# Kernel tuning notes

Hardware: AMD Instinct MI355X
Metric: run time of the kernel (lower is better)

Reference implementation:

```python
import jax, jax.numpy as jnp
import numpy as np

T, H, E, F = 2048, 1024, 32, 512   # tokens, hidden, routed experts, moe intermediate
K, NG, TG = 8, 8, 4                # top_k, n_group, topk_group
FS = 1024                          # shared-expert intermediate = n_shared(2) * F
SCALE = 2.5                        # routed_scaling_factor


def _silu_and_mul(gu):
    g, u = jnp.split(gu, 2, axis=-1)
    return jax.nn.silu(g) * u


def _route(x, gate_w, bias):
    # DeepSeek-V3 noaux_tc grouped top-k with correction bias (sigmoid scores)
    logits = x @ gate_w.T                                   # [T,E]
    scores = jax.nn.sigmoid(logits.astype(jnp.float32))
    sc = scores + bias[None, :]                             # biased scores, selection only
    n_tok = sc.shape[0]
    grp = sc.reshape(n_tok, NG, E // NG)
    top2, _ = jax.lax.top_k(grp, 2)
    group_scores = top2.sum(-1)                             # [T,NG]
    _, gidx = jax.lax.top_k(group_scores, TG)
    gmask = jnp.zeros((n_tok, NG), scores.dtype).at[jnp.arange(n_tok)[:, None], gidx].set(1.0)
    emask = jnp.repeat(gmask, E // NG, axis=1)              # [T,E]
    masked = jnp.where(emask > 0, sc, -jnp.inf)
    _, topk_idx = jax.lax.top_k(masked, K)                  # [T,K]
    w = jnp.take_along_axis(scores, topk_idx, axis=1)       # unbiased scores as weights
    w = w / (w.sum(-1, keepdims=True) + 1e-20)              # renormalize (norm_topk_prob)
    return w, topk_idx


def _forward(x, gate_w, corr_bias, w_gate_up, w_down, shared_gate_up, shared_down):
    w, idx = _route(x, gate_w, corr_bias)
    # dense grouped-GEMM reference: every expert on every token, sparse combine
    gu = jnp.einsum('th,egh->teg', x, w_gate_up)            # [T,E,2F]
    h = _silu_and_mul(gu)                                   # [T,E,F]
    y = jnp.einsum('tef,ehf->teh', h, w_down)               # [T,E,H]
    n_tok = x.shape[0]
    combine = jnp.zeros((n_tok, E), x.dtype).at[jnp.arange(n_tok)[:, None], idx].add(w.astype(x.dtype))
    routed = jnp.einsum('te,teh->th', combine, y) * SCALE
    shared = _silu_and_mul(x @ shared_gate_up.T) @ shared_down.T
    return routed + shared


def setup_inputs() -> dict:
    key = jax.random.key(0)
    ks = jax.random.split(key, 7)
    return {
        "hidden_states": jax.random.normal(ks[0], (T, H), jnp.float32),
        "gate_w": jax.random.normal(ks[1], (E, H), jnp.float32) * 0.02,
        "corr_bias": jax.random.normal(ks[2], (E,), jnp.float32) * 0.01,
        "w_gate_up": jax.random.normal(ks[3], (E, 2 * F, H), jnp.float32) * 0.02,
        "w_down": jax.random.normal(ks[4], (E, H, F), jnp.float32) * 0.02,
        "shared_gate_up": jax.random.normal(ks[5], (2 * FS, H), jnp.float32) * 0.02,
        "shared_down": jax.random.normal(ks[6], (H, FS), jnp.float32) * 0.02,
        "num_global_tokens": T,
        "max_num_tokens_per_gpu": T,
    }


def reference(hidden_states, gate_w, corr_bias, w_gate_up, w_down, shared_gate_up, shared_down, num_global_tokens, max_num_tokens_per_gpu):
    return _forward(hidden_states, gate_w, corr_bias, w_gate_up, w_down, shared_gate_up, shared_down)
```

## Files before the change

### kernel.cpp

```cpp
#include <hip/hip_runtime.h>
#include <hip/hip_bf16.h>

#define T_TOK 2048
#define H_DIM 1024
#define E_EXP 32
#define F_DIM 512
#define FS_DIM 1024
#define K_TOP 8
#define NGRP 8
#define TGRP 4
#define GSZ (E_EXP / NGRP)
#define RSCALE 2.5f
#define CAP 2048

typedef short  short8 __attribute__((ext_vector_type(8)));
typedef __bf16 bf16x4 __attribute__((ext_vector_type(4)));
typedef float  f32x4  __attribute__((ext_vector_type(4)));

__global__ void cvt_f32_bf16(const float* __restrict__ src, __bf16* __restrict__ dst, int n4) {
  int i = blockIdx.x * blockDim.x + threadIdx.x;
  const int stride = gridDim.x * blockDim.x;
  for (; i < n4; i += stride) {
    const float4 v = reinterpret_cast<const float4*>(src)[i];
    bf16x4 o;
    o[0] = (__bf16)v.x; o[1] = (__bf16)v.y; o[2] = (__bf16)v.z; o[3] = (__bf16)v.w;
    reinterpret_cast<bf16x4*>(dst)[i] = o;
  }
}

__global__ __launch_bounds__(64) void route_kernel(
    const float* __restrict__ x, const float* __restrict__ gw,
    const float* __restrict__ bias, int* __restrict__ tk_idx, float* __restrict__ tk_w) {
  const int t = blockIdx.x;
  const int lane = threadIdx.x;
  float xr[16];
#pragma unroll
  for (int i = 0; i < 16; i++) xr[i] = x[t * H_DIM + i * 64 + lane];
  float sc[E_EXP];
#pragma unroll
  for (int e = 0; e < E_EXP; e++) {
    const float* w = gw + e * H_DIM;
    float s = 0.f;
#pragma unroll
    for (int i = 0; i < 16; i++) s += xr[i] * w[i * 64 + lane];
#pragma unroll
    for (int off = 32; off > 0; off >>= 1) s += __shfl_xor(s, off);
    sc[e] = 1.f / (1.f + expf(-s));
  }
  if (lane == 0) {
    float b[E_EXP];
    for (int e = 0; e < E_EXP; e++) b[e] = sc[e] + bias[e];
    float gs[NGRP];
    for (int g = 0; g < NGRP; g++) {
      float m1 = -1e30f, m2 = -1e30f;
      for (int j = 0; j < GSZ; j++) {
        float v = b[g * GSZ + j];
        if (v > m1) { m2 = m1; m1 = v; } else if (v > m2) { m2 = v; }
      }
      gs[g] = m1 + m2;
    }
    unsigned gmask = 0;
    for (int it = 0; it < TGRP; it++) {
      float best = -1e30f; int bi = 0;
      for (int g = 0; g < NGRP; g++)
        if (!((gmask >> g) & 1) && gs[g] > best) { best = gs[g]; bi = g; }
      gmask |= 1u << bi;
    }
    unsigned emask = 0; float wsum = 0.f;
    int idx8[K_TOP];
    for (int it = 0; it < K_TOP; it++) {
      float best = -1e30f; int bi = 0;
      for (int e = 0; e < E_EXP; e++) {
        if (!((gmask >> (e / GSZ)) & 1)) continue;
        if ((emask >> e) & 1) continue;
        if (b[e] > best) { best = b[e]; bi = e; }
      }
      emask |= 1u << bi;
      idx8[it] = bi;
      wsum += sc[bi];
    }
    const float inv = 1.f / (wsum + 1e-20f);
    for (int k = 0; k < K_TOP; k++) {
      tk_idx[t * K_TOP + k] = idx8[k];
      tk_w[t * K_TOP + k] = sc[idx8[k]] * inv;
    }
  }
}

__global__ void scatter_kernel(const int* __restrict__ tk_idx, int* __restrict__ counts,
                               int* __restrict__ recs) {
  const int i = blockIdx.x * blockDim.x + threadIdx.x;
  if (i >= T_TOK * K_TOP) return;
  const int e = tk_idx[i];
  const int pos = atomicAdd(&counts[e], 1);
  recs[e * CAP + pos] = i;
}

__global__ void offsets_kernel(const int* __restrict__ counts, int* __restrict__ offs) {
  if (threadIdx.x == 0) {
    int a = 0;
    for (int e = 0; e < E_EXP; e++) { offs[e] = a; a += counts[e]; }
  }
}

#define BM 128
#define BN 128
#define BK 64

constexpr int MODE_GU = 0, MODE_DOWN = 1, MODE_SGU = 2, MODE_SDOWN = 3;

__device__ __forceinline__ void gload_lds16(const void* g, void* l) {
  __builtin_amdgcn_global_load_lds(
      (__attribute__((address_space(1))) const void*)g,
      (__attribute__((address_space(3))) void*)l, 16, 0, 0);
}

template <int MODE>
__global__ __launch_bounds__(256) void gemm_kernel(
    const __bf16* __restrict__ Abase, const __bf16* __restrict__ Bbase,
    void* __restrict__ Out,
    const int* __restrict__ recs, const int* __restrict__ counts,
    const int* __restrict__ offs, const float* __restrict__ tk_w) {

  constexpr int K = (MODE == MODE_DOWN) ? F_DIM : ((MODE == MODE_SDOWN) ? FS_DIM : H_DIM);

  const int e = (MODE == MODE_GU || MODE == MODE_DOWN) ? blockIdx.z : 0;
  const int m0 = blockIdx.y * BM;
  int count = T_TOK, off_e = 0;
  if (MODE == MODE_GU || MODE == MODE_DOWN) {
    count = counts[e];
    off_e = offs[e];
    if (m0 >= count) return;
  }
  const int tid = threadIdx.x, wid = tid >> 6, lane = tid & 63;

  __shared__ __align__(16) __bf16 As[BM * BK];
  __shared__ __align__(16) __bf16 Bs[BN * BK];

  const int colk = (lane & 7) * 8;
  const __bf16* aptr[4];
  const __bf16* bptr[4];
#pragma unroll
  for (int i = 0; i < 4; i++) {
    const int row = wid * 32 + i * 8 + (lane >> 3);
    if (MODE == MODE_GU) {
      int r = m0 + row; if (r > count - 1) r = count - 1;
      const int rec = recs[e * CAP + r];
      aptr[i] = Abase + (size_t)(rec >> 3) * H_DIM + colk;
    } else if (MODE == MODE_DOWN) {
      int r = m0 + row; if (r > count - 1) r = count - 1;
      aptr[i] = Abase + (size_t)(off_e + r) * F_DIM + colk;
    } else {
      aptr[i] = Abase + (size_t)(m0 + row) * K + colk;
    }
    int brow;
    if (MODE == MODE_GU)       brow = (row < 64) ? (blockIdx.x * 64 + row) : (F_DIM + blockIdx.x * 64 + row - 64);
    else if (MODE == MODE_SGU) brow = (row < 64) ? (blockIdx.x * 64 + row) : (FS_DIM + blockIdx.x * 64 + row - 64);
    else                       brow = blockIdx.x * BN + row;
    const __bf16* bexp = Bbase +
        ((MODE == MODE_GU)   ? (size_t)e * 2 * F_DIM * H_DIM :
         (MODE == MODE_DOWN) ? (size_t)e * H_DIM * F_DIM : (size_t)0);
    bptr[i] = bexp + (size_t)brow * K + colk;
  }

  f32x4 acc[2][8];
#pragma unroll
  for (int a = 0; a < 2; a++)
#pragma unroll
    for (int b = 0; b < 8; b++) acc[a][b] = f32x4{0.f, 0.f, 0.f, 0.f};

  const int lr = lane & 15, lh = lane >> 4;

  for (int k0 = 0; k0 < K; k0 += BK) {
#pragma unroll
    for (int i = 0; i < 4; i++)
      gload_lds16(aptr[i] + k0, (char*)As + (wid * 4 + i) * 1024);
#pragma unroll
    for (int i = 0; i < 4; i++)
      gload_lds16(bptr[i] + k0, (char*)Bs + (wid * 4 + i) * 1024);
    __syncthreads();
#pragma unroll
    for (int kk = 0; kk < 2; kk++) {
      short8 af[2], bfr[8];
#pragma unroll
      for (int fm = 0; fm < 2; fm++)
        af[fm] = *reinterpret_cast<const short8*>(&As[(wid * 32 + fm * 16 + lr) * BK + kk * 32 + lh * 8]);
#pragma unroll
      for (int fn = 0; fn < 8; fn++)
        bfr[fn] = *reinterpret_cast<const short8*>(&Bs[(fn * 16 + lr) * BK + kk * 32 + lh * 8]);
#pragma unroll
      for (int fn = 0; fn < 8; fn++)
#pragma unroll
        for (int fm = 0; fm < 2; fm++)
          acc[fm][fn] = __builtin_amdgcn_mfma_f32_16x16x32_bf16(af[fm], bfr[fn], acc[fm][fn], 0, 0, 0);
    }
    __syncthreads();
  }

  if (MODE == MODE_GU) {
    __bf16* h_out = (__bf16*)Out;
#pragma unroll
    for (int fm = 0; fm < 2; fm++)
#pragma unroll
      for (int j = 0; j < 4; j++) {
        const int row = wid * 32 + fm * 16 + lh * 4 + j;
        if (m0 + row < count) {
#pragma unroll
          for (int fn = 0; fn < 4; fn++) {
            const float g = acc[fm][fn][j], u = acc[fm][fn + 4][j];
            const float hv = g / (1.f + expf(-g)) * u;
            const int f = blockIdx.x * 64 + fn * 16 + lr;
            h_out[(size_t)(off_e + m0 + row) * F_DIM + f] = (__bf16)hv;
          }
        }
      }
  } else if (MODE == MODE_SGU) {
    __bf16* h_out = (__bf16*)Out;
#pragma unroll
    for (int fm = 0; fm < 2; fm++)
#pragma unroll
      for (int j = 0; j < 4; j++) {
        const int row = wid * 32 + fm * 16 + lh * 4 + j;
#pragma unroll
        for (int fn = 0; fn < 4; fn++) {
          const float g = acc[fm][fn][j], u = acc[fm][fn + 4][j];
          const float hv = g / (1.f + expf(-g)) * u;
          const int f = blockIdx.x * 64 + fn * 16 + lr;
          h_out[(size_t)(m0 + row) * FS_DIM + f] = (__bf16)hv;
        }
      }
  } else if (MODE == MODE_DOWN) {
    float* y = (float*)Out;
#pragma unroll
    for (int fm = 0; fm < 2; fm++)
#pragma unroll
      for (int j = 0; j < 4; j++) {
        const int row = wid * 32 + fm * 16 + lh * 4 + j;
        if (m0 + row < count) {
          const int rec = recs[e * CAP + m0 + row];
          const float w = tk_w[rec];
          const size_t base = (size_t)rec * H_DIM + blockIdx.x * BN;
#pragma unroll
          for (int fn = 0; fn < 8; fn++)
            y[base + fn * 16 + lr] = acc[fm][fn][j] * w;
        }
      }
  } else {
    float* o = (float*)Out;
#pragma unroll
    for (int fm = 0; fm < 2; fm++)
#pragma unroll
      for (int j = 0; j < 4; j++) {
        const int row = wid * 32 + fm * 16 + lh * 4 + j;
#pragma unroll
        for (int fn = 0; fn < 8; fn++)
          o[(size_t)(m0 + row) * H_DIM + blockIdx.x * BN + fn * 16 + lr] = acc[fm][fn][j];
      }
  }
}

__global__ void combine_kernel(const float* __restrict__ y_slot, float* __restrict__ out) {
  const int gid = blockIdx.x * blockDim.x + threadIdx.x;
  const int t = gid >> 8;
  const int c0 = (gid & 255) * 4;
  float4 s = {0.f, 0.f, 0.f, 0.f};
#pragma unroll
  for (int k = 0; k < K_TOP; k++) {
    const float4 v = *reinterpret_cast<const float4*>(&y_slot[((size_t)t * K_TOP + k) * H_DIM + c0]);
    s.x += v.x; s.y += v.y; s.z += v.z; s.w += v.w;
  }
  float4 o = *reinterpret_cast<float4*>(&out[(size_t)t * H_DIM + c0]);
  o.x += RSCALE * s.x; o.y += RSCALE * s.y; o.z += RSCALE * s.z; o.w += RSCALE * s.w;
  *reinterpret_cast<float4*>(&out[(size_t)t * H_DIM + c0]) = o;
}

extern "C" void kernel_launch(void* const* d_in, const int* in_sizes, int n_in,
                              void* d_out, int out_size, void* d_ws, size_t ws_size,
                              hipStream_t stream) {
  const float* x    = (const float*)d_in[0];
  const float* gw   = (const float*)d_in[1];
  const float* bias = (const float*)d_in[2];
  const float* wgu  = (const float*)d_in[3];
  const float* wd   = (const float*)d_in[4];
  const float* sgu  = (const float*)d_in[5];
  const float* sd   = (const float*)d_in[6];

  char* ws = (char*)d_ws;
  size_t o = 0;
  auto alloc = [&](size_t bytes) {
    char* p = ws + o;
    o += (bytes + 255) & ~(size_t)255;
    return (void*)p;
  };
  __bf16* xb     = (__bf16*)alloc((size_t)T_TOK * H_DIM * 2);
  __bf16* wgub   = (__bf16*)alloc((size_t)E_EXP * 2 * F_DIM * H_DIM * 2);
  __bf16* wdb    = (__bf16*)alloc((size_t)E_EXP * H_DIM * F_DIM * 2);
  __bf16* sgub   = (__bf16*)alloc((size_t)2 * FS_DIM * H_DIM * 2);
  __bf16* sdb    = (__bf16*)alloc((size_t)H_DIM * FS_DIM * 2);
  __bf16* h_buf  = (__bf16*)alloc((size_t)T_TOK * K_TOP * F_DIM * 2);
  float*  y_slot = (float*) alloc((size_t)T_TOK * K_TOP * H_DIM * 4);
  __bf16* hs     = (__bf16*)alloc((size_t)T_TOK * FS_DIM * 2);
  int*   tk_idx  = (int*)  alloc((size_t)T_TOK * K_TOP * 4);
  float* tk_w    = (float*)alloc((size_t)T_TOK * K_TOP * 4);
  int*   counts  = (int*)  alloc((size_t)E_EXP * 4);
  int*   offs    = (int*)  alloc((size_t)E_EXP * 4);
  int*   recs    = (int*)  alloc((size_t)E_EXP * CAP * 4);
  if (o > ws_size) return;

  cvt_f32_bf16<<<2048, 256, 0, stream>>>(x,   xb,   T_TOK * H_DIM / 4);
  cvt_f32_bf16<<<2048, 256, 0, stream>>>(wgu, wgub, E_EXP * 2 * F_DIM * H_DIM / 4);
  cvt_f32_bf16<<<2048, 256, 0, stream>>>(wd,  wdb,  E_EXP * H_DIM * F_DIM / 4);
  cvt_f32_bf16<<<2048, 256, 0, stream>>>(sgu, sgub, 2 * FS_DIM * H_DIM / 4);
  cvt_f32_bf16<<<1024, 256, 0, stream>>>(sd,  sdb,  H_DIM * FS_DIM / 4);

  route_kernel<<<T_TOK, 64, 0, stream>>>(x, gw, bias, tk_idx, tk_w);

  hipMemsetAsync(counts, 0, E_EXP * 4, stream);
  scatter_kernel<<<(T_TOK * K_TOP + 255) / 256, 256, 0, stream>>>(tk_idx, counts, recs);
  offsets_kernel<<<1, 64, 0, stream>>>(counts, offs);

  gemm_kernel<MODE_GU>   <<<dim3(F_DIM / 64, T_TOK / BM, E_EXP), 256, 0, stream>>>(xb, wgub, h_buf, recs, counts, offs, tk_w);
  gemm_kernel<MODE_DOWN> <<<dim3(H_DIM / BN, T_TOK / BM, E_EXP), 256, 0, stream>>>(h_buf, wdb, y_slot, recs, counts, offs, tk_w);
  gemm_kernel<MODE_SGU>  <<<dim3(FS_DIM / 64, T_TOK / BM, 1), 256, 0, stream>>>(xb, sgub, hs, recs, counts, offs, tk_w);
  gemm_kernel<MODE_SDOWN><<<dim3(H_DIM / BN, T_TOK / BM, 1), 256, 0, stream>>>(hs, sdb, d_out, recs, counts, offs, tk_w);

  combine_kernel<<<T_TOK * H_DIM / 4 / 256, 256, 0, stream>>>(y_slot, (float*)d_out);
}
```

Measured before the change: 318.8 us.

## Use 256x256 double-buffered tiles for routed expert GEMMs

Adds a separate 512-thread kernel for the routed gate-up and down GEMMs that uses 256x256 output tiles with an 8-wave 2x4 layout. It double-buffers the LDS tiles so the next K-slice loads while MFMAs run on the current one. The larger tiles are meant to raise arithmetic intensity and cut the number of blocks that reload the same weights. The shared-expert GEMMs keep the original 128x128 kernel. The cost is 128KB of LDS per block and heavy register pressure, which limits occupancy, and experts with few tokens may waste more work on partial tiles.

```diff
diff --git a/kernel.cpp b/kernel.cpp
--- a/kernel.cpp
+++ b/kernel.cpp
@@ -103,11 +103,7 @@
   }
 }
 
-#define BM 128
-#define BN 128
 #define BK 64
-
-constexpr int MODE_GU = 0, MODE_DOWN = 1, MODE_SGU = 2, MODE_SDOWN = 3;
 
 __device__ __forceinline__ void gload_lds16(const void* g, void* l) {
   __builtin_amdgcn_global_load_lds(
@@ -116,26 +112,25 @@
 }
 
 template <int MODE>
-__global__ __launch_bounds__(256) void gemm_kernel(
+__global__ __launch_bounds__(512, 2) void gemm256_kernel(
     const __bf16* __restrict__ Abase, const __bf16* __restrict__ Bbase,
     void* __restrict__ Out,
     const int* __restrict__ recs, const int* __restrict__ counts,
     const int* __restrict__ offs, const float* __restrict__ tk_w) {
 
-  constexpr int K = (MODE == MODE_DOWN) ? F_DIM : ((MODE == MODE_SDOWN) ? FS_DIM : H_DIM);
-
-  const int e = (MODE == MODE_GU || MODE == MODE_DOWN) ? blockIdx.z : 0;
-  const int m0 = blockIdx.y * BM;
-  int count = T_TOK, off_e = 0;
-  if (MODE == MODE_GU || MODE == MODE_DOWN) {
-    count = counts[e];
-    off_e = offs[e];
-    if (m0 >= count) return;
-  }
+  constexpr int K = (MODE == 0) ? H_DIM : F_DIM;
+  const int e = blockIdx.z;
+  const int m0 = blockIdx.y * 256;
+  const int count = counts[e];
+  const int off_e = offs[e];
+  if (m0 >= count) return;
+  const int bx = blockIdx.x;
   const int tid = threadIdx.x, wid = tid >> 6, lane = tid & 63;
-
-  __shared__ __align__(16) __bf16 As[BM * BK];
-  __shared__ __align__(16) __bf16 Bs[BN * BK];
+  const int wr = wid >> 2, wc = wid & 3;
+  const int lr = lane & 15, lh = lane >> 4;
+
+  __shared__ __align__(16) __bf16 As[2][256 * BK];
+  __shared__ __align__(16) __bf16 Bs[2][256 * BK];
 
   const int colk = (lane & 7) * 8;
   const __bf16* aptr[4];
@@ -143,24 +138,133 @@
 #pragma unroll
   for (int i = 0; i < 4; i++) {
     const int row = wid * 32 + i * 8 + (lane >> 3);
-    if (MODE == MODE_GU) {
-      int r = m0 + row; if (r > count - 1) r = count - 1;
+    int r = m0 + row; if (r > count - 1) r = count - 1;
+    if (MODE == 0) {
       const int rec = recs[e * CAP + r];
       aptr[i] = Abase + (size_t)(rec >> 3) * H_DIM + colk;
-    } else if (MODE == MODE_DOWN) {
-      int r = m0 + row; if (r > count - 1) r = count - 1;
+    } else {
       aptr[i] = Abase + (size_t)(off_e + r) * F_DIM + colk;
+    }
+    int brow;
+    if (MODE == 0) {
+      const int sub = row & 63, wcb = row >> 6;
+      const int f = bx * 128 + wcb * 32 + (sub & 31);
+      brow = (sub < 32) ? f : (F_DIM + f);
+      bptr[i] = Bbase + (size_t)e * 2 * F_DIM * H_DIM + (size_t)brow * H_DIM + colk;
     } else {
-      aptr[i] = Abase + (size_t)(m0 + row) * K + colk;
-    }
+      brow = bx * 256 + row;
+      bptr[i] = Bbase + (size_t)e * H_DIM * F_DIM + (size_t)brow * F_DIM + colk;
+    }
+  }
+
+  f32x4 acc[8][4];
+#pragma unroll
+  for (int a = 0; a < 8; a++)
+#pragma unroll
+    for (int b = 0; b < 4; b++) acc[a][b] = f32x4{0.f, 0.f, 0.f, 0.f};
+
+  constexpr int NT = K / BK;
+
+#pragma unroll
+  for (int i = 0; i < 4; i++) {
+    gload_lds16(aptr[i], (char*)&As[0][0] + (wid * 32 + i * 8) * 128);
+    gload_lds16(bptr[i], (char*)&Bs[0][0] + (wid * 32 + i * 8) * 128);
+  }
+  __syncthreads();
+
+  int cur = 0;
+  for (int t = 0; t < NT; ++t) {
+    if (t + 1 < NT) {
+      const int k0 = (t + 1) * BK;
+#pragma unroll
+      for (int i = 0; i < 4; i++) {
+        gload_lds16(aptr[i] + k0, (char*)&As[cur ^ 1][0] + (wid * 32 + i * 8) * 128);
+        gload_lds16(bptr[i] + k0, (char*)&Bs[cur ^ 1][0] + (wid * 32 + i * 8) * 128);
+      }
+    }
+#pragma unroll
+    for (int kk = 0; kk < 2; kk++) {
+      short8 af[8], bfr[4];
+#pragma unroll
+      for (int fm = 0; fm < 8; fm++)
+        af[fm] = *reinterpret_cast<const short8*>(&As[cur][(wr * 128 + fm * 16 + lr) * BK + kk * 32 + lh * 8]);
+#pragma unroll
+      for (int fn = 0; fn < 4; fn++)
+        bfr[fn] = *reinterpret_cast<const short8*>(&Bs[cur][(wc * 64 + fn * 16 + lr) * BK + kk * 32 + lh * 8]);
+#pragma unroll
+      for (int fn = 0; fn < 4; fn++)
+#pragma unroll
+        for (int fm = 0; fm < 8; fm++)
+          acc[fm][fn] = __builtin_amdgcn_mfma_f32_16x16x32_bf16(af[fm], bfr[fn], acc[fm][fn], 0, 0, 0);
+    }
+    __syncthreads();
+    cur ^= 1;
+  }
+
+  if (MODE == 0) {
+    __bf16* h_out = (__bf16*)Out;
+#pragma unroll
+    for (int fm = 0; fm < 8; fm++)
+#pragma unroll
+      for (int j = 0; j < 4; j++) {
+        const int row = wr * 128 + fm * 16 + lh * 4 + j;
+        if (m0 + row < count) {
+#pragma unroll
+          for (int fn = 0; fn < 2; fn++) {
+            const float g = acc[fm][fn][j], u = acc[fm][fn + 2][j];
+            const float hv = g / (1.f + expf(-g)) * u;
+            const int f = bx * 128 + wc * 32 + fn * 16 + lr;
+            h_out[(size_t)(off_e + m0 + row) * F_DIM + f] = (__bf16)hv;
+          }
+        }
+      }
+  } else {
+    float* y = (float*)Out;
+#pragma unroll
+    for (int fm = 0; fm < 8; fm++)
+#pragma unroll
+      for (int j = 0; j < 4; j++) {
+        const int row = wr * 128 + fm * 16 + lh * 4 + j;
+        if (m0 + row < count) {
+          const int rec = recs[e * CAP + m0 + row];
+          const float w = tk_w[rec];
+          const size_t base = (size_t)rec * H_DIM + bx * 256;
+#pragma unroll
+          for (int fn = 0; fn < 4; fn++)
+            y[base + wc * 64 + fn * 16 + lr] = acc[fm][fn][j] * w;
+        }
+      }
+  }
+}
+
+#define BM 128
+#define BN 128
+
+constexpr int MODE_SGU = 2, MODE_SDOWN = 3;
+
+template <int MODE>
+__global__ __launch_bounds__(256) void gemm_kernel(
+    const __bf16* __restrict__ Abase, const __bf16* __restrict__ Bbase,
+    void* __restrict__ Out) {
+
+  constexpr int K = (MODE == MODE_SDOWN) ? FS_DIM : H_DIM;
+  const int m0 = blockIdx.y * BM;
+  const int tid = threadIdx.x, wid = tid >> 6, lane = tid & 63;
+
+  __shared__ __align__(16) __bf16 As[BM * BK];
+  __shared__ __align__(16) __bf16 Bs[BN * BK];
+
+  const int colk = (lane & 7) * 8;
+  const __bf16* aptr[4];
+  const __bf16* bptr[4];
+#pragma unroll
+  for (int i = 0; i < 4; i++) {
+    const int row = wid * 32 + i * 8 + (lane >> 3);
+    aptr[i] = Abase + (size_t)(m0 + row) * K + colk;
     int brow;
-    if (MODE == MODE_GU)       brow = (row < 64) ? (blockIdx.x * 64 + row) : (F_DIM + blockIdx.x * 64 + row - 64);
-    else if (MODE == MODE_SGU) brow = (row < 64) ? (blockIdx.x * 64 + row) : (FS_DIM + blockIdx.x * 64 + row - 64);
-    else                       brow = blockIdx.x * BN + row;
-    const __bf16* bexp = Bbase +
-        ((MODE == MODE_GU)   ? (size_t)e * 2 * F_DIM * H_DIM :
-         (MODE == MODE_DOWN) ? (size_t)e * H_DIM * F_DIM : (size_t)0);
-    bptr[i] = bexp + (size_t)brow * K + colk;
+    if (MODE == MODE_SGU) brow = (row < 64) ? (blockIdx.x * 64 + row) : (FS_DIM + blockIdx.x * 64 + row - 64);
+    else                  brow = blockIdx.x * BN + row;
+    bptr[i] = Bbase + (size_t)brow * K + colk;
   }
 
   f32x4 acc[2][8];
@@ -197,24 +301,7 @@
     __syncthreads();
   }
 
-  if (MODE == MODE_GU) {
-    __bf16* h_out = (__bf16*)Out;
-#pragma unroll
-    for (int fm = 0; fm < 2; fm++)
-#pragma unroll
-      for (int j = 0; j < 4; j++) {
-        const int row = wid * 32 + fm * 16 + lh * 4 + j;
-        if (m0 + row < count) {
-#pragma unroll
-          for (int fn = 0; fn < 4; fn++) {
-            const float g = acc[fm][fn][j], u = acc[fm][fn + 4][j];
-            const float hv = g / (1.f + expf(-g)) * u;
-            const int f = blockIdx.x * 64 + fn * 16 + lr;
-            h_out[(size_t)(off_e + m0 + row) * F_DIM + f] = (__bf16)hv;
-          }
-        }
-      }
-  } else if (MODE == MODE_SGU) {
+  if (MODE == MODE_SGU) {
     __bf16* h_out = (__bf16*)Out;
 #pragma unroll
     for (int fm = 0; fm < 2; fm++)
@@ -227,22 +314,6 @@
           const float hv = g / (1.f + expf(-g)) * u;
           const int f = blockIdx.x * 64 + fn * 16 + lr;
           h_out[(size_t)(m0 + row) * FS_DIM + f] = (__bf16)hv;
-        }
-      }
-  } else if (MODE == MODE_DOWN) {
-    float* y = (float*)Out;
-#pragma unroll
-    for (int fm = 0; fm < 2; fm++)
-#pragma unroll
-      for (int j = 0; j < 4; j++) {
-        const int row = wid * 32 + fm * 16 + lh * 4 + j;
-        if (m0 + row < count) {
-          const int rec = recs[e * CAP + m0 + row];
-          const float w = tk_w[rec];
-          const size_t base = (size_t)rec * H_DIM + blockIdx.x * BN;
-#pragma unroll
-          for (int fn = 0; fn < 8; fn++)
-            y[base + fn * 16 + lr] = acc[fm][fn][j] * w;
         }
       }
   } else {
@@ -319,10 +390,10 @@
   scatter_kernel<<<(T_TOK * K_TOP + 255) / 256, 256, 0, stream>>>(tk_idx, counts, recs);
   offsets_kernel<<<1, 64, 0, stream>>>(counts, offs);
 
-  gemm_kernel<MODE_GU>   <<<dim3(F_DIM / 64, T_TOK / BM, E_EXP), 256, 0, stream>>>(xb, wgub, h_buf, recs, counts, offs, tk_w);
-  gemm_kernel<MODE_DOWN> <<<dim3(H_DIM / BN, T_TOK / BM, E_EXP), 256, 0, stream>>>(h_buf, wdb, y_slot, recs, counts, offs, tk_w);
-  gemm_kernel<MODE_SGU>  <<<dim3(FS_DIM / 64, T_TOK / BM, 1), 256, 0, stream>>>(xb, sgub, hs, recs, counts, offs, tk_w);
-  gemm_kernel<MODE_SDOWN><<<dim3(H_DIM / BN, T_TOK / BM, 1), 256, 0, stream>>>(hs, sdb, d_out, recs, counts, offs, tk_w);
+  gemm256_kernel<0><<<dim3(2 * F_DIM / 256, CAP / 256, E_EXP), 512, 0, stream>>>(xb, wgub, h_buf, recs, counts, offs, tk_w);
+  gemm256_kernel<1><<<dim3(H_DIM / 256, CAP / 256, E_EXP), 512, 0, stream>>>(h_buf, wdb, y_slot, recs, counts, offs, tk_w);
+  gemm_kernel<MODE_SGU>  <<<dim3(FS_DIM / 64, T_TOK / BM), 256, 0, stream>>>(xb, sgub, hs);
+  gemm_kernel<MODE_SDOWN><<<dim3(H_DIM / BN, T_TOK / BM), 256, 0, stream>>>(hs, sdb, d_out);
 
   combine_kernel<<<T_TOK * H_DIM / 4 / 256, 256, 0, stream>>>(y_slot, (float*)d_out);
 }
```

Result: slower. 557.0 us (+74.7%).

## Merge routed and shared GEMMs into shared launches and fold scatter into routing

Applied to the files above, without the earlier changes.

Combines the five conversion launches into one kernel and moves the x conversion into the routing kernel. The expert scatter (atomic counts and record lists) now happens inside routing, which removes the scatter and offsets kernels; each GEMM block instead computes its prefix offset from the counts. Routed and shared-expert GEMMs run in the same launch per phase by using extra z slices, so the dense shared work can fill gaps left by the uneven expert tiles. The cost is more branching inside the GEMM, a prefix sum per block, and atomics issued by one lane per token.

```diff
diff --git a/kernel.cpp b/kernel.cpp
--- a/kernel.cpp
+++ b/kernel.cpp
@@ -17,10 +17,24 @@
 typedef __bf16 bf16x4 __attribute__((ext_vector_type(4)));
 typedef float  f32x4  __attribute__((ext_vector_type(4)));
 
-__global__ void cvt_f32_bf16(const float* __restrict__ src, __bf16* __restrict__ dst, int n4) {
-  int i = blockIdx.x * blockDim.x + threadIdx.x;
+__global__ void cvt_all(const float* __restrict__ s0, __bf16* __restrict__ d0, int n0,
+                        const float* __restrict__ s1, __bf16* __restrict__ d1, int n1,
+                        const float* __restrict__ s2, __bf16* __restrict__ d2, int n2,
+                        const float* __restrict__ s3, __bf16* __restrict__ d3, int n3) {
+  const int ntot = n0 + n1 + n2 + n3;
+  int gid = blockIdx.x * blockDim.x + threadIdx.x;
   const int stride = gridDim.x * blockDim.x;
-  for (; i < n4; i += stride) {
+  for (; gid < ntot; gid += stride) {
+    int i = gid;
+    const float* src; __bf16* dst;
+    if (i < n0) { src = s0; dst = d0; }
+    else { i -= n0;
+      if (i < n1) { src = s1; dst = d1; }
+      else { i -= n1;
+        if (i < n2) { src = s2; dst = d2; }
+        else { i -= n2; src = s3; dst = d3; }
+      }
+    }
     const float4 v = reinterpret_cast<const float4*>(src)[i];
     bf16x4 o;
     o[0] = (__bf16)v.x; o[1] = (__bf16)v.y; o[2] = (__bf16)v.z; o[3] = (__bf16)v.w;
@@ -30,12 +44,15 @@
 
 __global__ __launch_bounds__(64) void route_kernel(
     const float* __restrict__ x, const float* __restrict__ gw,
-    const float* __restrict__ bias, int* __restrict__ tk_idx, float* __restrict__ tk_w) {
+    const float* __restrict__ bias, float* __restrict__ tk_w,
+    int* __restrict__ counts, int* __restrict__ recs, __bf16* __restrict__ xb) {
   const int t = blockIdx.x;
   const int lane = threadIdx.x;
   float xr[16];
 #pragma unroll
   for (int i = 0; i < 16; i++) xr[i] = x[t * H_DIM + i * 64 + lane];
+#pragma unroll
+  for (int i = 0; i < 16; i++) xb[t * H_DIM + i * 64 + lane] = (__bf16)xr[i];
   float sc[E_EXP];
 #pragma unroll
   for (int e = 0; e < E_EXP; e++) {
@@ -81,33 +98,17 @@
     }
     const float inv = 1.f / (wsum + 1e-20f);
     for (int k = 0; k < K_TOP; k++) {
-      tk_idx[t * K_TOP + k] = idx8[k];
-      tk_w[t * K_TOP + k] = sc[idx8[k]] * inv;
-    }
-  }
-}
-
-__global__ void scatter_kernel(const int* __restrict__ tk_idx, int* __restrict__ counts,
-                               int* __restrict__ recs) {
-  const int i = blockIdx.x * blockDim.x + threadIdx.x;
-  if (i >= T_TOK * K_TOP) return;
-  const int e = tk_idx[i];
-  const int pos = atomicAdd(&counts[e], 1);
-  recs[e * CAP + pos] = i;
-}
-
-__global__ void offsets_kernel(const int* __restrict__ counts, int* __restrict__ offs) {
-  if (threadIdx.x == 0) {
-    int a = 0;
-    for (int e = 0; e < E_EXP; e++) { offs[e] = a; a += counts[e]; }
+      const int e = idx8[k];
+      tk_w[t * K_TOP + k] = sc[e] * inv;
+      const int pos = atomicAdd(&counts[e], 1);
+      recs[e * CAP + pos] = t * K_TOP + k;
+    }
   }
 }
 
 #define BM 128
 #define BN 128
 #define BK 64
-
-constexpr int MODE_GU = 0, MODE_DOWN = 1, MODE_SGU = 2, MODE_SDOWN = 3;
 
 __device__ __forceinline__ void gload_lds16(const void* g, void* l) {
   __builtin_amdgcn_global_load_lds(
@@ -115,27 +116,32 @@
       (__attribute__((address_space(3))) void*)l, 16, 0, 0);
 }
 
-template <int MODE>
-__global__ __launch_bounds__(256) void gemm_kernel(
-    const __bf16* __restrict__ Abase, const __bf16* __restrict__ Bbase,
-    void* __restrict__ Out,
+template <int PHASE>
+__global__ __launch_bounds__(256) void gemm_fused(
+    const __bf16* __restrict__ Ar, const __bf16* __restrict__ As_,
+    const __bf16* __restrict__ Br, const __bf16* __restrict__ Bs_,
+    void* __restrict__ OutR, void* __restrict__ OutS,
     const int* __restrict__ recs, const int* __restrict__ counts,
-    const int* __restrict__ offs, const float* __restrict__ tk_w) {
-
-  constexpr int K = (MODE == MODE_DOWN) ? F_DIM : ((MODE == MODE_SDOWN) ? FS_DIM : H_DIM);
-
-  const int e = (MODE == MODE_GU || MODE == MODE_DOWN) ? blockIdx.z : 0;
+    const float* __restrict__ tk_w) {
+
+  const int z = blockIdx.z;
+  const bool routed = (z < E_EXP);
+  const int e = z;
   const int m0 = blockIdx.y * BM;
+  const int bx = blockIdx.x;
+
   int count = T_TOK, off_e = 0;
-  if (MODE == MODE_GU || MODE == MODE_DOWN) {
+  if (routed) {
     count = counts[e];
-    off_e = offs[e];
+    for (int i = 0; i < E_EXP; i++) off_e += (i < e) ? counts[i] : 0;
     if (m0 >= count) return;
   }
+  const int K = (PHASE == 0) ? H_DIM : (routed ? F_DIM : FS_DIM);
+
   const int tid = threadIdx.x, wid = tid >> 6, lane = tid & 63;
 
-  __shared__ __align__(16) __bf16 As[BM * BK];
-  __shared__ __align__(16) __bf16 Bs[BN * BK];
+  __shared__ __align__(16) __bf16 Atile[BM * BK];
+  __shared__ __align__(16) __bf16 Btile[BN * BK];
 
   const int colk = (lane & 7) * 8;
   const __bf16* aptr[4];
@@ -143,24 +149,37 @@
 #pragma unroll
   for (int i = 0; i < 4; i++) {
     const int row = wid * 32 + i * 8 + (lane >> 3);
-    if (MODE == MODE_GU) {
-      int r = m0 + row; if (r > count - 1) r = count - 1;
-      const int rec = recs[e * CAP + r];
-      aptr[i] = Abase + (size_t)(rec >> 3) * H_DIM + colk;
-    } else if (MODE == MODE_DOWN) {
-      int r = m0 + row; if (r > count - 1) r = count - 1;
-      aptr[i] = Abase + (size_t)(off_e + r) * F_DIM + colk;
+    int r = m0 + row; if (r > count - 1) r = count - 1;
+    if (PHASE == 0) {
+      if (routed) {
+        const int rec = recs[e * CAP + r];
+        aptr[i] = Ar + (size_t)(rec >> 3) * H_DIM + colk;
+      } else {
+        aptr[i] = As_ + (size_t)r * H_DIM + colk;
+      }
     } else {
-      aptr[i] = Abase + (size_t)(m0 + row) * K + colk;
-    }
-    int brow;
-    if (MODE == MODE_GU)       brow = (row < 64) ? (blockIdx.x * 64 + row) : (F_DIM + blockIdx.x * 64 + row - 64);
-    else if (MODE == MODE_SGU) brow = (row < 64) ? (blockIdx.x * 64 + row) : (FS_DIM + blockIdx.x * 64 + row - 64);
-    else                       brow = blockIdx.x * BN + row;
-    const __bf16* bexp = Bbase +
-        ((MODE == MODE_GU)   ? (size_t)e * 2 * F_DIM * H_DIM :
-         (MODE == MODE_DOWN) ? (size_t)e * H_DIM * F_DIM : (size_t)0);
-    bptr[i] = bexp + (size_t)brow * K + colk;
+      if (routed) aptr[i] = Ar + (size_t)(off_e + r) * F_DIM + colk;
+      else        aptr[i] = As_ + (size_t)r * FS_DIM + colk;
+    }
+    if (PHASE == 0) {
+      if (routed) {
+        const int brow = (row < 64) ? (bx * 64 + row) : (F_DIM + bx * 64 + row - 64);
+        bptr[i] = Br + (size_t)e * 2 * F_DIM * H_DIM + (size_t)brow * H_DIM + colk;
+      } else {
+        const int s = z - E_EXP;
+        const int fglob = s * 512 + bx * 64 + (row & 63);
+        const int brow = (row < 64) ? fglob : (FS_DIM + fglob);
+        bptr[i] = Bs_ + (size_t)brow * H_DIM + colk;
+      }
+    } else {
+      if (routed) {
+        const int brow = bx * BN + row;
+        bptr[i] = Br + (size_t)e * H_DIM * F_DIM + (size_t)brow * F_DIM + colk;
+      } else {
+        const int brow = bx * BN + row;
+        bptr[i] = Bs_ + (size_t)brow * FS_DIM + colk;
+      }
+    }
   }
 
   f32x4 acc[2][8];
@@ -174,20 +193,20 @@
   for (int k0 = 0; k0 < K; k0 += BK) {
 #pragma unroll
     for (int i = 0; i < 4; i++)
-      gload_lds16(aptr[i] + k0, (char*)As + (wid * 4 + i) * 1024);
+      gload_lds16(aptr[i] + k0, (char*)Atile + (wid * 4 + i) * 1024);
 #pragma unroll
     for (int i = 0; i < 4; i++)
-      gload_lds16(bptr[i] + k0, (char*)Bs + (wid * 4 + i) * 1024);
+      gload_lds16(bptr[i] + k0, (char*)Btile + (wid * 4 + i) * 1024);
     __syncthreads();
 #pragma unroll
     for (int kk = 0; kk < 2; kk++) {
       short8 af[2], bfr[8];
 #pragma unroll
       for (int fm = 0; fm < 2; fm++)
-        af[fm] = *reinterpret_cast<const short8*>(&As[(wid * 32 + fm * 16 + lr) * BK + kk * 32 + lh * 8]);
+        af[fm] = *reinterpret_cast<const short8*>(&Atile[(wid * 32 + fm * 16 + lr) * BK + kk * 32 + lh * 8]);
 #pragma unroll
       for (int fn = 0; fn < 8; fn++)
-        bfr[fn] = *reinterpret_cast<const short8*>(&Bs[(fn * 16 + lr) * BK + kk * 32 + lh * 8]);
+        bfr[fn] = *reinterpret_cast<const short8*>(&Btile[(fn * 16 + lr) * BK + kk * 32 + lh * 8]);
 #pragma unroll
       for (int fn = 0; fn < 8; fn++)
 #pragma unroll
@@ -197,8 +216,7 @@
     __syncthreads();
   }
 
-  if (MODE == MODE_GU) {
-    __bf16* h_out = (__bf16*)Out;
+  if (PHASE == 0) {
 #pragma unroll
     for (int fm = 0; fm < 2; fm++)
 #pragma unroll
@@ -209,52 +227,37 @@
           for (int fn = 0; fn < 4; fn++) {
             const float g = acc[fm][fn][j], u = acc[fm][fn + 4][j];
             const float hv = g / (1.f + expf(-g)) * u;
-            const int f = blockIdx.x * 64 + fn * 16 + lr;
-            h_out[(size_t)(off_e + m0 + row) * F_DIM + f] = (__bf16)hv;
+            if (routed) {
+              const int f = bx * 64 + fn * 16 + lr;
+              ((__bf16*)OutR)[(size_t)(off_e + m0 + row) * F_DIM + f] = (__bf16)hv;
+            } else {
+              const int s = z - E_EXP;
+              const int f = s * 512 + bx * 64 + fn * 16 + lr;
+              ((__bf16*)OutS)[(size_t)(m0 + row) * FS_DIM + f] = (__bf16)hv;
+            }
           }
         }
       }
-  } else if (MODE == MODE_SGU) {
-    __bf16* h_out = (__bf16*)Out;
-#pragma unroll
-    for (int fm = 0; fm < 2; fm++)
-#pragma unroll
-      for (int j = 0; j < 4; j++) {
-        const int row = wid * 32 + fm * 16 + lh * 4 + j;
-#pragma unroll
-        for (int fn = 0; fn < 4; fn++) {
-          const float g = acc[fm][fn][j], u = acc[fm][fn + 4][j];
-          const float hv = g / (1.f + expf(-g)) * u;
-          const int f = blockIdx.x * 64 + fn * 16 + lr;
-          h_out[(size_t)(m0 + row) * FS_DIM + f] = (__bf16)hv;
-        }
-      }
-  } else if (MODE == MODE_DOWN) {
-    float* y = (float*)Out;
+  } else {
 #pragma unroll
     for (int fm = 0; fm < 2; fm++)
 #pragma unroll
       for (int j = 0; j < 4; j++) {
         const int row = wid * 32 + fm * 16 + lh * 4 + j;
         if (m0 + row < count) {
-          const int rec = recs[e * CAP + m0 + row];
-          const float w = tk_w[rec];
-          const size_t base = (size_t)rec * H_DIM + blockIdx.x * BN;
-#pragma unroll
-          for (int fn = 0; fn < 8; fn++)
-            y[base + fn * 16 + lr] = acc[fm][fn][j] * w;
+          if (routed) {
+            const int rec = recs[e * CAP + m0 + row];
+            const float w = tk_w[rec];
+            const size_t base = (size_t)rec * H_DIM + bx * BN;
+#pragma unroll
+            for (int fn = 0; fn < 8; fn++)
+              ((float*)OutR)[base + fn * 16 + lr] = acc[fm][fn][j] * w;
+          } else {
+#pragma unroll
+            for (int fn = 0; fn < 8; fn++)
+              ((float*)OutS)[(size_t)(m0 + row) * H_DIM + bx * BN + fn * 16 + lr] = acc[fm][fn][j];
+          }
         }
-      }
-  } else {
-    float* o = (float*)Out;
-#pragma unroll
-    for (int fm = 0; fm < 2; fm++)
-#pragma unroll
-      for (int j = 0; j < 4; j++) {
-        const int row = wid * 32 + fm * 16 + lh * 4 + j;
-#pragma unroll
-        for (int fn = 0; fn < 8; fn++)
-          o[(size_t)(m0 + row) * H_DIM + blockIdx.x * BN + fn * 16 + lr] = acc[fm][fn][j];
       }
   }
 }
@@ -300,29 +303,25 @@
   __bf16* h_buf  = (__bf16*)alloc((size_t)T_TOK * K_TOP * F_DIM * 2);
   float*  y_slot = (float*) alloc((size_t)T_TOK * K_TOP * H_DIM * 4);
   __bf16* hs     = (__bf16*)alloc((size_t)T_TOK * FS_DIM * 2);
-  int*   tk_idx  = (int*)  alloc((size_t)T_TOK * K_TOP * 4);
   float* tk_w    = (float*)alloc((size_t)T_TOK * K_TOP * 4);
   int*   counts  = (int*)  alloc((size_t)E_EXP * 4);
-  int*   offs    = (int*)  alloc((size_t)E_EXP * 4);
   int*   recs    = (int*)  alloc((size_t)E_EXP * CAP * 4);
   if (o > ws_size) return;
 
-  cvt_f32_bf16<<<2048, 256, 0, stream>>>(x,   xb,   T_TOK * H_DIM / 4);
-  cvt_f32_bf16<<<2048, 256, 0, stream>>>(wgu, wgub, E_EXP * 2 * F_DIM * H_DIM / 4);
-  cvt_f32_bf16<<<2048, 256, 0, stream>>>(wd,  wdb,  E_EXP * H_DIM * F_DIM / 4);
-  cvt_f32_bf16<<<2048, 256, 0, stream>>>(sgu, sgub, 2 * FS_DIM * H_DIM / 4);
-  cvt_f32_bf16<<<1024, 256, 0, stream>>>(sd,  sdb,  H_DIM * FS_DIM / 4);
-
-  route_kernel<<<T_TOK, 64, 0, stream>>>(x, gw, bias, tk_idx, tk_w);
+  cvt_all<<<2048, 256, 0, stream>>>(
+      wgu, wgub, E_EXP * 2 * F_DIM * H_DIM / 4,
+      wd,  wdb,  E_EXP * H_DIM * F_DIM / 4,
+      sgu, sgub, 2 * FS_DIM * H_DIM / 4,
+      sd,  sdb,  H_DIM * FS_DIM / 4);
 
   hipMemsetAsync(counts, 0, E_EXP * 4, stream);
-  scatter_kernel<<<(T_TOK * K_TOP + 255) / 256, 256, 0, stream>>>(tk_idx, counts, recs);
-  offsets_kernel<<<1, 64, 0, stream>>>(counts, offs);
-
-  gemm_kernel<MODE_GU>   <<<dim3(F_DIM / 64, T_TOK / BM, E_EXP), 256, 0, stream>>>(xb, wgub, h_buf, recs, counts, offs, tk_w);
-  gemm_kernel<MODE_DOWN> <<<dim3(H_DIM / BN, T_TOK / BM, E_EXP), 256, 0, stream>>>(h_buf, wdb, y_slot, recs, counts, offs, tk_w);
-  gemm_kernel<MODE_SGU>  <<<dim3(FS_DIM / 64, T_TOK / BM, 1), 256, 0, stream>>>(xb, sgub, hs, recs, counts, offs, tk_w);
-  gemm_kernel<MODE_SDOWN><<<dim3(H_DIM / BN, T_TOK / BM, 1), 256, 0, stream>>>(hs, sdb, d_out, recs, counts, offs, tk_w);
+  route_kernel<<<T_TOK, 64, 0, stream>>>(x, gw, bias, tk_w, counts, recs, xb);
+
+  gemm_fused<0><<<dim3(F_DIM / 64, T_TOK / BM, E_EXP + 2), 256, 0, stream>>>(
+      xb, xb, wgub, sgub, h_buf, hs, recs, counts, tk_w);
+
+  gemm_fused<1><<<dim3(H_DIM / BN, T_TOK / BM, E_EXP + 1), 256, 0, stream>>>(
+      h_buf, hs, wdb, sdb, y_slot, d_out, recs, counts, tk_w);
 
   combine_kernel<<<T_TOK * H_DIM / 4 / 256, 256, 0, stream>>>(y_slot, (float*)d_out);
 }
```

Result: slower. 364.0 us (+14.2%).
